# Kernel tuning notes

Hardware: AMD Instinct MI355X
Metric: run time of the kernel (lower is better)

Reference implementation:

```python
import jax, jax.numpy as jnp
import numpy as np


def setup_inputs() -> dict:
    key = jax.random.key(0)
    k1, k2 = jax.random.split(key)
    N, K, D = 32768, 8192, 256
    inputs = jax.random.normal(k1, (N, D), dtype=jnp.float32)
    embedding = jax.random.normal(k2, (K, D), dtype=jnp.float32)  # codebook buffer
    return {"inputs": inputs, "embedding": embedding}


def reference(inputs, embedding):
    # distances[n, k] = ||x_n||^2 + ||e_k||^2 - 2 <x_n, e_k>   (squared L2, as in torch source)
    x_sq = jnp.sum(inputs * inputs, axis=1, keepdims=True)          # [N, 1]
    e_sq = jnp.sum(embedding * embedding, axis=1)                   # [K]
    cross = inputs @ embedding.T                                    # [N, K]
    distances = x_sq + e_sq - 2.0 * cross                           # [N, K]
    encoding_indices = jnp.argmin(distances, axis=1)                # [N] int
    # torch forward returns (None, None, indices); return the tensor output
    return encoding_indices
```

## Files before the change

kernel.cpp:

```cpp
#include <hip/hip_runtime.h>

constexpr int D_DIM   = 256;
constexpr int N_ROWS  = 32768;
constexpr int K_CODES = 8192;
constexpr unsigned TQ = 58;

typedef _Float16 f16x8  __attribute__((ext_vector_type(8)));
typedef __fp16   fp16x2 __attribute__((ext_vector_type(2)));
typedef float    f32x16 __attribute__((ext_vector_type(16)));

#define MFMA32(a, b, c) __builtin_amdgcn_mfma_f32_32x32x16_f16(a, b, c, 0, 0, 0)

__device__ __forceinline__ void cvt_rtn(const float4 a, const float4 b,
                                        uint4& hi, uint4& lo) {
    float f[8] = {a.x, a.y, a.z, a.w, b.x, b.y, b.z, b.w};
    unsigned hb[8], lb[8];
#pragma unroll
    for (int i = 0; i < 8; ++i) {
        _Float16 h = (_Float16)f[i];
        _Float16 l = (_Float16)(f[i] - (float)h);
        hb[i] = __builtin_bit_cast(unsigned short, h);
        lb[i] = __builtin_bit_cast(unsigned short, l);
    }
    hi = make_uint4(hb[0] | (hb[1] << 16), hb[2] | (hb[3] << 16),
                    hb[4] | (hb[5] << 16), hb[6] | (hb[7] << 16));
    lo = make_uint4(lb[0] | (lb[1] << 16), lb[2] | (lb[3] << 16),
                    lb[4] | (lb[5] << 16), lb[6] | (lb[7] << 16));
}

__device__ __forceinline__ void cvt_granule(const float4 a, const float4 b,
                                            uint4& hi, uint4& lo) {
    fp16x2 h0 = __builtin_amdgcn_cvt_pkrtz(a.x, a.y);
    fp16x2 h1 = __builtin_amdgcn_cvt_pkrtz(a.z, a.w);
    fp16x2 h2 = __builtin_amdgcn_cvt_pkrtz(b.x, b.y);
    fp16x2 h3 = __builtin_amdgcn_cvt_pkrtz(b.z, b.w);
    fp16x2 l0 = __builtin_amdgcn_cvt_pkrtz(a.x - (float)h0.x, a.y - (float)h0.y);
    fp16x2 l1 = __builtin_amdgcn_cvt_pkrtz(a.z - (float)h1.x, a.w - (float)h1.y);
    fp16x2 l2 = __builtin_amdgcn_cvt_pkrtz(b.x - (float)h2.x, b.y - (float)h2.y);
    fp16x2 l3 = __builtin_amdgcn_cvt_pkrtz(b.z - (float)h3.x, b.w - (float)h3.y);
    hi = make_uint4(__builtin_bit_cast(unsigned, h0), __builtin_bit_cast(unsigned, h1),
                    __builtin_bit_cast(unsigned, h2), __builtin_bit_cast(unsigned, h3));
    lo = make_uint4(__builtin_bit_cast(unsigned, l0), __builtin_bit_cast(unsigned, l1),
                    __builtin_bit_cast(unsigned, l2), __builtin_bit_cast(unsigned, l3));
}

__device__ __forceinline__ void gl_lds16(const uint4* g, uint4* l) {
    __builtin_amdgcn_global_load_lds(
        (const __attribute__((address_space(1))) void*)g,
        (__attribute__((address_space(3))) void*)l, 16, 0, 0);
}

__global__ __launch_bounds__(256)
void prep_kernel(const float* __restrict__ X, const float* __restrict__ E,
                 uint4* __restrict__ Xh,
                 uint4* __restrict__ Eh, uint4* __restrict__ El,
                 float* __restrict__ esqb, int* __restrict__ cnt) {
    const int tid = threadIdx.x, bid = blockIdx.x;
    if (bid < 1024) {
#pragma unroll 1
        for (int it = 0; it < 4; ++it) {
            const int gid = bid * 1024 + it * 256 + tid;
            const int rb = gid >> 12, rem = gid & 4095;
            const int Lg = rem >> 7, r = rem & 127;
            const float* p = X + (size_t)(rb * 128 + r) * D_DIM + Lg * 8;
            const float4 a = *(const float4*)p, b = *(const float4*)(p + 4);
            uint4 hi, lo; cvt_rtn(a, b, hi, lo);
            Xh[gid] = hi;
        }
    } else if (bid < 1280) {
#pragma unroll 1
        for (int it = 0; it < 4; ++it) {
            const int gid = (bid - 1024) * 1024 + it * 256 + tid;
            const int cb = gid >> 13, rem = gid & 8191;
            const int Lg = rem >> 8, c = rem & 255;
            const float* p = E + (size_t)(cb * 256 + c) * D_DIM + Lg * 8;
            const float4 a = *(const float4*)p, b = *(const float4*)(p + 4);
            uint4 hi, lo; cvt_rtn(a, b, hi, lo);
            Eh[gid] = hi; El[gid] = lo;
        }
    } else {
        if (bid == 1280 && tid == 0) *cnt = 0;
        const int t = (bid - 1280) * 256 + tid;
        const int gw = t >> 6, lane = t & 63;
        const float4 v = ((const float4*)(E + (size_t)gw * D_DIM))[lane];
        float s = v.x * v.x + v.y * v.y + v.z * v.z + v.w * v.w;
#pragma unroll
        for (int off = 32; off; off >>= 1) s += __shfl_down(s, off, 64);
        if (lane == 0) esqb[gw] = s + 1024.0f;
    }
}

__global__ __launch_bounds__(256, 2)
void vq_pass1(const uint4* __restrict__ Xh, const uint4* __restrict__ Eh,
              const float* __restrict__ esqb, uint2* __restrict__ res) {
    __shared__ uint4 sXh[4096];
    __shared__ uint2 slot[2][128];

    const int tid  = threadIdx.x;
    const int lane = tid & 63, wv = tid >> 6, wr = wv >> 1, wc = wv & 1;
    const int l31  = lane & 31, lh = lane >> 5;
    const int wbase = wv << 6;
    const int bx = blockIdx.x, strip = blockIdx.y;
    const int cs0 = strip * 2048;

    const uint4* Xhb = Xh + bx * 4096;

#pragma unroll
    for (int i = 0; i < 16; ++i)
        gl_lds16(Xhb + i * 256 + tid, &sXh[i * 256 + wbase]);
    __syncthreads();

    unsigned best[2][16], best2[2][16];
#pragma unroll
    for (int ti = 0; ti < 2; ++ti)
#pragma unroll
        for (int r = 0; r < 16; ++r) { best[ti][r] = 0xFFFFFFFFu; best2[ti][r] = 0xFFFFFFFFu; }

    f32x16 acc[2][2];
    const int arow = wr * 64 + l31;

#pragma unroll 1
    for (int ct = 0; ct < 16; ++ct) {
        const uint4* __restrict__ Eb =
            Eh + (size_t)(strip * 8 + (ct >> 1)) * 8192 + (ct & 1) * 128 + wc * 64 + l31;

#pragma unroll
        for (int ti = 0; ti < 2; ++ti)
#pragma unroll
            for (int tj = 0; tj < 2; ++tj)
#pragma unroll
                for (int i = 0; i < 16; ++i) acc[ti][tj][i] = 0.0f;

#pragma unroll 4
        for (int k = 0; k < 16; ++k) {
            const int Lg = k * 2 + lh;
            const f16x8 b0 = __builtin_bit_cast(f16x8, Eb[Lg * 256]);
            const f16x8 b1 = __builtin_bit_cast(f16x8, Eb[Lg * 256 + 32]);
            const f16x8 a0 = __builtin_bit_cast(f16x8, sXh[Lg * 128 + arow]);
            const f16x8 a1 = __builtin_bit_cast(f16x8, sXh[Lg * 128 + arow + 32]);
            acc[0][0] = MFMA32(a0, b0, acc[0][0]);
            acc[0][1] = MFMA32(a0, b1, acc[0][1]);
            acc[1][0] = MFMA32(a1, b0, acc[1][0]);
            acc[1][1] = MFMA32(a1, b1, acc[1][1]);
        }

#pragma unroll
        for (int tj = 0; tj < 2; ++tj) {
            const int code = cs0 + ct * 128 + wc * 64 + tj * 32 + l31;
            const float eb128 = esqb[code] * 128.0f;
#pragma unroll
            for (int ti = 0; ti < 2; ++ti)
#pragma unroll
                for (int r = 0; r < 16; ++r) {
                    const float dq = fmaf(-256.0f, acc[ti][tj][r], eb128);
                    const unsigned q   = (unsigned)dq;
                    const unsigned key = (q << 13) + (unsigned)code;
                    const unsigned t   = key > best[ti][r] ? key : best[ti][r];
                    best2[ti][r] = best2[ti][r] < t ? best2[ti][r] : t;
                    best[ti][r]  = best[ti][r] < key ? best[ti][r] : key;
                }
        }
    }

#pragma unroll
    for (int ti = 0; ti < 2; ++ti)
#pragma unroll
        for (int r = 0; r < 16; ++r) {
            unsigned b1 = best[ti][r], b2 = best2[ti][r];
#pragma unroll
            for (int m = 16; m >= 1; m >>= 1) {
                const unsigned o1 = (unsigned)__shfl_xor((int)b1, m, 32);
                const unsigned o2 = (unsigned)__shfl_xor((int)b2, m, 32);
                const unsigned t  = b1 > o1 ? b1 : o1;
                b1 = b1 < o1 ? b1 : o1;
                const unsigned m2 = b2 < o2 ? b2 : o2;
                b2 = m2 < t ? m2 : t;
            }
            if (l31 == 0) {
                const int row = wr * 64 + ti * 32 + (r & 3) + 8 * (r >> 2) + 4 * lh;
                slot[wc][row] = make_uint2(b1, b2);
            }
        }

    __syncthreads();
    if (tid < 128) {
        const uint2 A = slot[0][tid], B = slot[1][tid];
        const unsigned t  = A.x > B.x ? A.x : B.x;
        const unsigned b1 = A.x < B.x ? A.x : B.x;
        const unsigned m2 = A.y < B.y ? A.y : B.y;
        const unsigned b2 = m2 < t ? m2 : t;
        res[(size_t)strip * N_ROWS + bx * 128 + tid] = make_uint2(b1, b2);
    }
}

__global__ void merge_kernel(const uint2* __restrict__ res,
                             unsigned long long* __restrict__ res0,
                             int* __restrict__ out,
                             int* __restrict__ cnt, int* __restrict__ list) {
    const int row = blockIdx.x * 256 + threadIdx.x;
    unsigned b1 = 0xFFFFFFFFu, b2 = 0xFFFFFFFFu;
#pragma unroll
    for (int s = 0; s < 4; ++s) {
        const uint2 v = res[(size_t)s * N_ROWS + row];
        const unsigned t = b1 > v.x ? b1 : v.x;
        b1 = b1 < v.x ? b1 : v.x;
        const unsigned m2 = b2 < v.y ? b2 : v.y;
        b2 = m2 < t ? m2 : t;
    }
    out[row] = (int)(b1 & 8191u);
    if ((b2 >> 13) - (b1 >> 13) < TQ) {
        const int p = atomicAdd(cnt, 1);
        list[p] = row;
        res0[row] = ~0ull;
    }
}

__global__ __launch_bounds__(256, 1)
void refine_kernel(const float* __restrict__ X,
                   const uint4* __restrict__ Eh, const uint4* __restrict__ El,
                   const float* __restrict__ esqb, const int* __restrict__ cnt,
                   const int* __restrict__ list, unsigned long long* __restrict__ res0) {
    __shared__ int  rows_s[32];
    __shared__ uint4 sAh[1024], sAl[1024];

    const int n = *cnt;
    const int base = blockIdx.x * 32;
    if (base >= n) return;
    const int tid = threadIdx.x;
    if (tid < 32) { const int j = base + tid; rows_s[tid] = list[j < n ? j : base]; }
    __syncthreads();

#pragma unroll
    for (int jj = 0; jj < 4; ++jj) {
        const int gg = jj * 256 + tid, Lg = gg >> 5, rr = gg & 31;
        const int row = rows_s[rr];
        const float* p = X + (size_t)row * D_DIM + Lg * 8;
        const float4 a = *(const float4*)p, b = *(const float4*)(p + 4);
        uint4 hi, lo; cvt_rtn(a, b, hi, lo);
        sAh[Lg * 32 + rr] = hi; sAl[Lg * 32 + rr] = lo;
    }
    __syncthreads();

    const int lane = tid & 63, wv = tid >> 6, l31 = lane & 31, lh = lane >> 5;
    const int cbase = blockIdx.y * 1024 + wv * 256;

    float bestv[16]; int besti[16];
#pragma unroll
    for (int r = 0; r < 16; ++r) { bestv[r] = 3.0e38f; besti[r] = 0; }

#pragma unroll 1
    for (int ps = 0; ps < 2; ++ps) {
        const int c0 = cbase + ps * 128;
        f32x16 acc[4];
#pragma unroll
        for (int tj = 0; tj < 4; ++tj)
#pragma unroll
            for (int i = 0; i < 16; ++i) acc[tj][i] = 0.0f;

#pragma unroll
        for (int ks = 0; ks < 16; ++ks) {
            const int Lg = ks * 2 + lh;
            f16x8 b0[4], b1[4];
#pragma unroll
            for (int tj = 0; tj < 4; ++tj) {
                const int c = c0 + tj * 32 + l31;
                const int eg = (c >> 8) * 8192 + Lg * 256 + (c & 255);
                b0[tj] = __builtin_bit_cast(f16x8, Eh[eg]);
                b1[tj] = __builtin_bit_cast(f16x8, El[eg]);
            }
            const f16x8 a0 = __builtin_bit_cast(f16x8, sAh[Lg * 32 + l31]);
            const f16x8 a1 = __builtin_bit_cast(f16x8, sAl[Lg * 32 + l31]);
#pragma unroll
            for (int tj = 0; tj < 4; ++tj) acc[tj] = MFMA32(a1, b0[tj], acc[tj]);
#pragma unroll
            for (int tj = 0; tj < 4; ++tj) acc[tj] = MFMA32(a0, b1[tj], acc[tj]);
#pragma unroll
            for (int tj = 0; tj < 4; ++tj) acc[tj] = MFMA32(a0, b0[tj], acc[tj]);
        }

#pragma unroll
        for (int tj = 0; tj < 4; ++tj) {
            const int c = c0 + tj * 32 + l31;
            const float eb = esqb[c];
#pragma unroll
            for (int r = 0; r < 16; ++r) {
                const float dv = fmaf(-2.0f, acc[tj][r], eb);
                if (dv < bestv[r]) { bestv[r] = dv; besti[r] = c; }
            }
        }
    }

#pragma unroll
    for (int r = 0; r < 16; ++r) {
        float v = bestv[r]; int bi = besti[r];
#pragma unroll
        for (int m = 16; m >= 1; m >>= 1) {
            const float ov = __shfl_xor(v, m, 32);
            const int   oi = __shfl_xor(bi, m, 32);
            if (ov < v || (ov == v && oi < bi)) { v = ov; bi = oi; }
        }
        if (l31 == 0) {
            const int rl = (r & 3) + 8 * (r >> 2) + 4 * lh;
            atomicMin(&res0[rows_s[rl]],
                      ((unsigned long long)__float_as_uint(v) << 32) | (unsigned)bi);
        }
    }
}

__global__ void finalize_kernel(const unsigned long long* __restrict__ res0,
                                const int* __restrict__ cnt, const int* __restrict__ list,
                                int* __restrict__ out) {
    const int i = blockIdx.x * 256 + threadIdx.x;
    if (i < *cnt) {
        const int row = list[i];
        out[row] = (int)(res0[row] & 0xFFFFFFFFull);
    }
}

__global__ void prologue_fb(const float* __restrict__ E, float* __restrict__ esqb,
                            unsigned long long* __restrict__ packed) {
    const int t = blockIdx.x * 256 + threadIdx.x;
    if (t < N_ROWS) packed[t] = ~0ull;
    const int gw = t >> 6, lane = t & 63;
    const float4 v = ((const float4*)(E + (size_t)gw * D_DIM))[lane];
    float s = v.x * v.x + v.y * v.y + v.z * v.z + v.w * v.w;
#pragma unroll
    for (int off = 32; off; off >>= 1) s += __shfl_down(s, off, 64);
    if (lane == 0) esqb[gw] = s + 1024.0f;
}

__global__ __launch_bounds__(256, 2)
void vq_mfma_fallback(const float* __restrict__ X, const float* __restrict__ E,
                      const float* __restrict__ esqb,
                      unsigned long long* __restrict__ packed) {
    __shared__ uint4 fXh[128 * 8], fXl[128 * 8];
    __shared__ uint4 fEh[128 * 8], fEl[128 * 8];
    __shared__ float fEsq[2048];

    const int tid  = threadIdx.x;
    const int lane = tid & 63;
    const int wv   = tid >> 6;
    const int wr   = wv >> 1, wc = wv & 1;
    const int l31  = lane & 31;
    const int lh   = lane >> 5;
    const int row0 = blockIdx.x * 128;
    const int cs0  = blockIdx.y * 2048;

#pragma unroll
    for (int i = 0; i < 8; ++i) fEsq[tid + 256 * i] = esqb[cs0 + tid + 256 * i];

    const int sr = tid >> 3, sg = tid & 7;

    float best[2][16]; int bidx[2][16];
#pragma unroll
    for (int ti = 0; ti < 2; ++ti)
#pragma unroll
        for (int r = 0; r < 16; ++r) { best[ti][r] = 3.0e38f; bidx[ti][r] = 0; }

    f32x16 acc[2][2];

#pragma unroll 1
    for (int ct = 0; ct < 16; ++ct) {
#pragma unroll
        for (int ti = 0; ti < 2; ++ti)
#pragma unroll
            for (int tj = 0; tj < 2; ++tj)
#pragma unroll
                for (int i = 0; i < 16; ++i) acc[ti][tj][i] = 0.0f;

#pragma unroll 1
        for (int dc = 0; dc < 4; ++dc) {
            __syncthreads();
#pragma unroll
            for (int i = 0; i < 4; ++i) {
                const int r = 32 * i + sr;
                const float* p = X + (size_t)(row0 + r) * D_DIM + dc * 64 + sg * 8;
                const float4 a = *(const float4*)p, b = *(const float4*)(p + 4);
                uint4 hi, lo; cvt_granule(a, b, hi, lo);
                const int o = r * 8 + (sg ^ (r & 7));
                fXh[o] = hi; fXl[o] = lo;
            }
#pragma unroll
            for (int i = 0; i < 4; ++i) {
                const int r = 32 * i + sr;
                const float* p = E + (size_t)(cs0 + ct * 128 + r) * D_DIM + dc * 64 + sg * 8;
                const float4 a = *(const float4*)p, b = *(const float4*)(p + 4);
                uint4 hi, lo; cvt_granule(a, b, hi, lo);
                const int o = r * 8 + (sg ^ (r & 7));
                fEh[o] = hi; fEl[o] = lo;
            }
            __syncthreads();

#pragma unroll
            for (int s = 0; s < 4; ++s) {
                const int gi = s * 2 + lh;
                f16x8 axh[2], axl[2], beh[2], bel[2];
#pragma unroll
                for (int ti = 0; ti < 2; ++ti) {
                    const int r = wr * 64 + ti * 32 + l31;
                    const int o = r * 8 + (gi ^ (r & 7));
                    axh[ti] = __builtin_bit_cast(f16x8, fXh[o]);
                    axl[ti] = __builtin_bit_cast(f16x8, fXl[o]);
                }
#pragma unroll
                for (int tj = 0; tj < 2; ++tj) {
                    const int c = wc * 64 + tj * 32 + l31;
                    const int o = c * 8 + (gi ^ (c & 7));
                    beh[tj] = __builtin_bit_cast(f16x8, fEh[o]);
                    bel[tj] = __builtin_bit_cast(f16x8, fEl[o]);
                }
#pragma unroll
                for (int ti = 0; ti < 2; ++ti)
#pragma unroll
                    for (int tj = 0; tj < 2; ++tj) {
                        acc[ti][tj] = MFMA32(axl[ti], beh[tj], acc[ti][tj]);
                        acc[ti][tj] = MFMA32(axh[ti], bel[tj], acc[ti][tj]);
                        acc[ti][tj] = MFMA32(axh[ti], beh[tj], acc[ti][tj]);
                    }
            }
        }

#pragma unroll
        for (int tj = 0; tj < 2; ++tj) {
            const int cloc = ct * 128 + wc * 64 + tj * 32 + l31;
            const float eb = fEsq[cloc];
            const int  code = cs0 + cloc;
#pragma unroll
            for (int ti = 0; ti < 2; ++ti)
#pragma unroll
                for (int r = 0; r < 16; ++r) {
                    const float dv = fmaf(-2.0f, acc[ti][tj][r], eb);
                    if (dv < best[ti][r]) { best[ti][r] = dv; bidx[ti][r] = code; }
                }
        }
    }

#pragma unroll
    for (int ti = 0; ti < 2; ++ti)
#pragma unroll
        for (int r = 0; r < 16; ++r) {
            float b = best[ti][r]; int bi = bidx[ti][r];
#pragma unroll
            for (int m = 16; m >= 1; m >>= 1) {
                const float ov = __shfl_xor(b, m, 32);
                const int   oi = __shfl_xor(bi, m, 32);
                if (ov < b || (ov == b && oi < bi)) { b = ov; bi = oi; }
            }
            if (l31 == 0) {
                const int row = row0 + wr * 64 + ti * 32 + (r & 3) + 8 * (r >> 2) + 4 * lh;
                const unsigned long long p =
                    ((unsigned long long)__float_as_uint(b) << 32) | (unsigned)bi;
                atomicMin(&packed[row], p);
            }
        }
}

__global__ void finish_fb(const unsigned long long* __restrict__ packed,
                          int* __restrict__ out) {
    const int i = blockIdx.x * 256 + threadIdx.x;
    out[i] = (int)(unsigned)(packed[i] & 0xffffffffull);
}

extern "C" void kernel_launch(void* const* d_in, const int* in_sizes, int n_in,
                              void* d_out, int out_size, void* d_ws, size_t ws_size,
                              hipStream_t stream) {
    const float* X = (const float*)d_in[0];
    const float* E = (const float*)d_in[1];
    char* ws = (char*)d_ws;
    int* out = (int*)d_out;

    float* esqb = (float*)ws;
    uint2* res  = (uint2*)(ws + 32768);
    unsigned long long* res0 = (unsigned long long*)(ws + 1081344);
    int* cnt  = (int*)(ws + 1343488);
    int* list = (int*)(ws + 1343504);
    const size_t base = 1572864;
    const size_t szX  = (size_t)N_ROWS * D_DIM * 2;
    const size_t szE  = (size_t)K_CODES * D_DIM * 2;
    const size_t need = base + szX + 2 * szE;

    if (ws_size >= need) {
        uint4* Xh = (uint4*)(ws + base);
        uint4* Eh = (uint4*)(ws + base + szX);
        uint4* El = (uint4*)(ws + base + szX + szE);
        prep_kernel<<<dim3(3328), dim3(256), 0, stream>>>(X, E, Xh, Eh, El, esqb, cnt);
        vq_pass1<<<dim3(N_ROWS / 128, 4), dim3(256), 0, stream>>>(Xh, Eh, esqb, res);
        merge_kernel<<<dim3(N_ROWS / 256), dim3(256), 0, stream>>>(res, res0, out, cnt, list);
        refine_kernel<<<dim3(1024, 8), dim3(256), 0, stream>>>(X, Eh, El, esqb,
                                                               cnt, list, res0);
        finalize_kernel<<<dim3(N_ROWS / 256), dim3(256), 0, stream>>>(res0, cnt, list, out);
    } else {
        unsigned long long* packed = (unsigned long long*)(ws + 32768);
        prologue_fb<<<dim3(2048), dim3(256), 0, stream>>>(E, esqb, packed);
        vq_mfma_fallback<<<dim3(N_ROWS / 128, 4), dim3(256), 0, stream>>>(X, E, esqb, packed);
        finish_fb<<<dim3(N_ROWS / 256), dim3(256), 0, stream>>>(packed, out);
    }
}
```

Measured before the change: 360.9 us.

## Shrink pass1 row tile to 64 with 4 column-waves and med3 top-2 update

Changes the pass-1 block tile from 128 rows × 128 codes per step (2×2 waves) to 64 rows × 256 codes (4 waves along codes). The prep layout for Xh and the LDS footprint are halved to match, and the launch is now a flattened 2048-block grid with occupancy hint 3. The top-2 tracking is reduced to a v_med3_u32 plus a min. The aim is higher occupancy and a cheaper epilogue, at the cost of less reuse of E loads across rows, so global/L2 traffic for the codebook doubles.

```diff
diff --git a/kernel.cpp b/kernel.cpp
--- a/kernel.cpp
+++ b/kernel.cpp
@@ -60,9 +60,9 @@
 #pragma unroll 1
         for (int it = 0; it < 4; ++it) {
             const int gid = bid * 1024 + it * 256 + tid;
-            const int rb = gid >> 12, rem = gid & 4095;
-            const int Lg = rem >> 7, r = rem & 127;
-            const float* p = X + (size_t)(rb * 128 + r) * D_DIM + Lg * 8;
+            const int rb = gid >> 11, rem = gid & 2047;
+            const int Lg = rem >> 6, r = rem & 63;
+            const float* p = X + (size_t)(rb * 64 + r) * D_DIM + Lg * 8;
             const float4 a = *(const float4*)p, b = *(const float4*)(p + 4);
             uint4 hi, lo; cvt_rtn(a, b, hi, lo);
             Xh[gid] = hi;
@@ -90,24 +90,24 @@
     }
 }
 
-__global__ __launch_bounds__(256, 2)
+__global__ __launch_bounds__(256, 3)
 void vq_pass1(const uint4* __restrict__ Xh, const uint4* __restrict__ Eh,
               const float* __restrict__ esqb, uint2* __restrict__ res) {
-    __shared__ uint4 sXh[4096];
-    __shared__ uint2 slot[2][128];
+    __shared__ uint4 sXh[2048];
+    __shared__ uint2 slot[4][64];
 
     const int tid  = threadIdx.x;
-    const int lane = tid & 63, wv = tid >> 6, wr = wv >> 1, wc = wv & 1;
+    const int lane = tid & 63, wv = tid >> 6;
     const int l31  = lane & 31, lh = lane >> 5;
-    const int wbase = wv << 6;
-    const int bx = blockIdx.x, strip = blockIdx.y;
+    const int bid  = blockIdx.x;
+    const int bx = bid & 511, strip = bid >> 9;
     const int cs0 = strip * 2048;
 
-    const uint4* Xhb = Xh + bx * 4096;
-
-#pragma unroll
-    for (int i = 0; i < 16; ++i)
-        gl_lds16(Xhb + i * 256 + tid, &sXh[i * 256 + wbase]);
+    const uint4* Xhb = Xh + bx * 2048;
+
+#pragma unroll
+    for (int i = 0; i < 8; ++i)
+        gl_lds16(Xhb + i * 256 + tid, &sXh[i * 256 + (wv << 6)]);
     __syncthreads();
 
     unsigned best[2][16], best2[2][16];
@@ -117,12 +117,11 @@
         for (int r = 0; r < 16; ++r) { best[ti][r] = 0xFFFFFFFFu; best2[ti][r] = 0xFFFFFFFFu; }
 
     f32x16 acc[2][2];
-    const int arow = wr * 64 + l31;
 
 #pragma unroll 1
-    for (int ct = 0; ct < 16; ++ct) {
+    for (int ct = 0; ct < 8; ++ct) {
         const uint4* __restrict__ Eb =
-            Eh + (size_t)(strip * 8 + (ct >> 1)) * 8192 + (ct & 1) * 128 + wc * 64 + l31;
+            Eh + (size_t)(strip * 8 + ct) * 8192 + wv * 64 + l31;
 
 #pragma unroll
         for (int ti = 0; ti < 2; ++ti)
@@ -136,8 +135,8 @@
             const int Lg = k * 2 + lh;
             const f16x8 b0 = __builtin_bit_cast(f16x8, Eb[Lg * 256]);
             const f16x8 b1 = __builtin_bit_cast(f16x8, Eb[Lg * 256 + 32]);
-            const f16x8 a0 = __builtin_bit_cast(f16x8, sXh[Lg * 128 + arow]);
-            const f16x8 a1 = __builtin_bit_cast(f16x8, sXh[Lg * 128 + arow + 32]);
+            const f16x8 a0 = __builtin_bit_cast(f16x8, sXh[Lg * 64 + l31]);
+            const f16x8 a1 = __builtin_bit_cast(f16x8, sXh[Lg * 64 + l31 + 32]);
             acc[0][0] = MFMA32(a0, b0, acc[0][0]);
             acc[0][1] = MFMA32(a0, b1, acc[0][1]);
             acc[1][0] = MFMA32(a1, b0, acc[1][0]);
@@ -146,7 +145,7 @@
 
 #pragma unroll
         for (int tj = 0; tj < 2; ++tj) {
-            const int code = cs0 + ct * 128 + wc * 64 + tj * 32 + l31;
+            const int code = cs0 + ct * 256 + wv * 64 + tj * 32 + l31;
             const float eb128 = esqb[code] * 128.0f;
 #pragma unroll
             for (int ti = 0; ti < 2; ++ti)
@@ -155,9 +154,12 @@
                     const float dq = fmaf(-256.0f, acc[ti][tj][r], eb128);
                     const unsigned q   = (unsigned)dq;
                     const unsigned key = (q << 13) + (unsigned)code;
-                    const unsigned t   = key > best[ti][r] ? key : best[ti][r];
-                    best2[ti][r] = best2[ti][r] < t ? best2[ti][r] : t;
-                    best[ti][r]  = best[ti][r] < key ? best[ti][r] : key;
+                    unsigned nb2;
+                    asm("v_med3_u32 %0, %1, %2, %3"
+                        : "=v"(nb2)
+                        : "v"(key), "v"(best[ti][r]), "v"(best2[ti][r]));
+                    best2[ti][r] = nb2;
+                    best[ti][r]  = key < best[ti][r] ? key : best[ti][r];
                 }
         }
     }
@@ -177,19 +179,24 @@
                 b2 = m2 < t ? m2 : t;
             }
             if (l31 == 0) {
-                const int row = wr * 64 + ti * 32 + (r & 3) + 8 * (r >> 2) + 4 * lh;
-                slot[wc][row] = make_uint2(b1, b2);
+                const int row = ti * 32 + (r & 3) + 8 * (r >> 2) + 4 * lh;
+                slot[wv][row] = make_uint2(b1, b2);
             }
         }
 
     __syncthreads();
-    if (tid < 128) {
-        const uint2 A = slot[0][tid], B = slot[1][tid];
-        const unsigned t  = A.x > B.x ? A.x : B.x;
-        const unsigned b1 = A.x < B.x ? A.x : B.x;
-        const unsigned m2 = A.y < B.y ? A.y : B.y;
-        const unsigned b2 = m2 < t ? m2 : t;
-        res[(size_t)strip * N_ROWS + bx * 128 + tid] = make_uint2(b1, b2);
+    if (tid < 64) {
+        const uint2 A = slot[0][tid];
+        unsigned b1 = A.x, b2 = A.y;
+#pragma unroll
+        for (int s = 1; s < 4; ++s) {
+            const uint2 B = slot[s][tid];
+            const unsigned t  = b1 > B.x ? b1 : B.x;
+            b1 = b1 < B.x ? b1 : B.x;
+            const unsigned m2 = b2 < B.y ? b2 : B.y;
+            b2 = m2 < t ? m2 : t;
+        }
+        res[(size_t)strip * N_ROWS + bx * 64 + tid] = make_uint2(b1, b2);
     }
 }
 
@@ -484,7 +491,7 @@
         uint4* Eh = (uint4*)(ws + base + szX);
         uint4* El = (uint4*)(ws + base + szX + szE);
         prep_kernel<<<dim3(3328), dim3(256), 0, stream>>>(X, E, Xh, Eh, El, esqb, cnt);
-        vq_pass1<<<dim3(N_ROWS / 128, 4), dim3(256), 0, stream>>>(Xh, Eh, esqb, res);
+        vq_pass1<<<dim3(2048), dim3(256), 0, stream>>>(Xh, Eh, esqb, res);
         merge_kernel<<<dim3(N_ROWS / 256), dim3(256), 0, stream>>>(res, res0, out, cnt, list);
         refine_kernel<<<dim3(1024, 8), dim3(256), 0, stream>>>(X, Eh, El, esqb,
                                                                cnt, list, res0);
```

Result: faster. 327.7 us (-9.2%).
